# Optimization experiments

Hardware: AMD Instinct MI355X
Metric: run time of the kernel (lower is better)

The kernel has to match this reference:

```python
import jax, jax.numpy as jnp
import numpy as np
import math

BLKQ = 64
BLKK = 32
TOPK_FRAC = 0.1


def setup_inputs() -> dict:
    key = jax.random.key(0)
    k1, k2, k3, k4, k5 = jax.random.split(key, 5)
    B, L, H, D = 1, 8192, 16, 64
    q = jax.random.normal(k1, (B, L, H, D), jnp.float32)
    k = jax.random.normal(k2, (B, L, H, D), jnp.float32)
    v = jax.random.normal(k3, (B, L, H, D), jnp.float32)
    # proj_l initialized with nn.init.normal_ (std=1) in the original
    W_proj = jax.random.normal(k4, (D, D), jnp.float32)
    b_proj = jax.random.normal(k5, (D,), jnp.float32)
    return {"q": q, "k": k, "v": v, "W_proj": W_proj, "b_proj": b_proj}


def reference(q, k, v, W_proj, b_proj):
    B, L, H, D = q.shape
    lcm = BLKQ * BLKK // math.gcd(BLKQ, BLKK)
    L_pad = ((L + lcm - 1) // lcm) * lcm
    pad = L_pad - L
    scale = 1.0 / math.sqrt(D)

    # [B, L, H, D] -> [B, H, L_pad, D], zero padded (fused_transpose_pad)
    qt = jnp.transpose(q, (0, 2, 1, 3))
    kt = jnp.transpose(k, (0, 2, 1, 3))
    vt = jnp.transpose(v, (0, 2, 1, 3))
    if pad:
        pw = ((0, 0), (0, 0), (0, pad), (0, 0))
        qt_p = jnp.pad(qt, pw); kt_p = jnp.pad(kt, pw); vt_p = jnp.pad(vt, pw)
    else:
        qt_p, kt_p, vt_p = qt, kt, vt

    # key smoothing (SAGE): subtract per-(b,h) mean of padded k
    km = kt_p.mean(axis=-2, keepdims=True)          # [B, H, 1, D]
    kc = kt_p - km

    M = L_pad // BLKQ
    N = L_pad // BLKK
    # block pooling for routing scores
    pooled_q = qt_p.reshape(B, H, M, BLKQ, D).mean(axis=3)   # [B,H,M,D]
    pooled_k = kc.reshape(B, H, N, BLKK, D).mean(axis=3)     # [B,H,N,D]
    score = jnp.einsum('bhmd,bhnd->bhmn', pooled_q, pooled_k)

    T = min(N, int(TOPK_FRAC * N))                  # real_topk (static)
    _, idx = jax.lax.top_k(score, T)                # [B,H,M,T]
    lut = jnp.sort(idx, axis=-1)

    # gather selected key/value blocks: [B,H,M,T,BLKK,D]
    kb = kc.reshape(B, H, N, BLKK, D)
    vb = vt_p.reshape(B, H, N, BLKK, D)
    kg = jnp.take_along_axis(kb[:, :, None], lut[..., None, None], axis=3)
    vg = jnp.take_along_axis(vb[:, :, None], lut[..., None, None], axis=3)

    qb = qt_p.reshape(B, H, M, BLKQ, D)
    # block-sparse scores: [B,H,M,BLKQ,T,BLKK]
    s = jnp.einsum('bhmqd,bhmtkd->bhmqtk', qb, kg) * scale
    key_pos = lut[..., None] * BLKK + jnp.arange(BLKK)       # [B,H,M,T,BLKK]
    valid = key_pos < L
    s = jnp.where(valid[:, :, :, None, :, :], s, -jnp.inf)
    s = s.reshape(B, H, M, BLKQ, T * BLKK)
    p = jax.nn.softmax(s, axis=-1)
    o_s = jnp.einsum('bhmqn,bhmnd->bhmqd', p, vg.reshape(B, H, M, T * BLKK, D))
    o_s = o_s.reshape(B, H, L_pad, D)[:, :, :L]              # slice to seq_len

    # linear attention branch (softmax feature map over D)
    q_fm = jax.nn.softmax(qt_p[:, :, :L], axis=-1)
    k_fm = jax.nn.softmax(kt_p[:, :, :L], axis=-1)
    kvsum = jnp.einsum('bhld,bhle->bhde', k_fm, vt)          # [B,H,D,D]
    ksum = k_fm.sum(axis=-2)                                 # [B,H,D]
    denom = jnp.einsum('bhld,bhd->bhl', q_fm, ksum)[..., None] + 1e-6
    o_l = jnp.einsum('bhld,bhde->bhle', q_fm, kvsum) / denom
    o_l = o_l @ W_proj.T + b_proj                            # proj_l

    o = jnp.transpose(o_l + o_s, (0, 2, 1, 3))               # [B,L,H,D]
    return o
```

## Files before the change

kernel.cpp:

```cpp
#include <hip/hip_runtime.h>
#include <math.h>

#define SEQL 8192
#define NH 16
#define HD 1024
#define TSEL 25

#define OFF_KVPART 0
#define OFF_KSUM   262144
#define OFF_ZEND   263168
#define OFF_PK     263168
#define OFF_KWT    525312
#define OFF_KSWZ   558080
#define OFF_LUT    131072

typedef __attribute__((ext_vector_type(8))) short bf16x8;
typedef __attribute__((ext_vector_type(4))) float f32x4;

static __device__ inline short f2bf(float f) {
    union { float f; unsigned u; } c; c.f = f;
    unsigned r = (c.u + 0x7FFFu + ((c.u >> 16) & 1u)) >> 16;
    return (short)r;
}
static __device__ inline bf16x8 cvt8(float4 a, float4 b) {
    bf16x8 r;
    r[0] = f2bf(a.x); r[1] = f2bf(a.y); r[2] = f2bf(a.z); r[3] = f2bf(a.w);
    r[4] = f2bf(b.x); r[5] = f2bf(b.y); r[6] = f2bf(b.z); r[7] = f2bf(b.w);
    return r;
}
static __device__ inline unsigned cvtpk(float a, float b) {
    unsigned r;
    asm("v_cvt_pk_bf16_f32 %0, %1, %2" : "=v"(r) : "v"(a), "v"(b));
    return r;
}
static __device__ inline float exp2a(float x) {
#if __has_builtin(__builtin_amdgcn_exp2f)
    return __builtin_amdgcn_exp2f(x);
#else
    float r; asm("v_exp_f32 %0, %1" : "=v"(r) : "v"(x)); return r;
#endif
}
static __device__ inline void load_lds16(const void* g, void* l) {
    __builtin_amdgcn_global_load_lds((const __attribute__((address_space(1))) unsigned int*)g,
                                     (__attribute__((address_space(3))) unsigned int*)l,
                                     16, 0, 0);
}

__global__ __launch_bounds__(256) void prep_lin(const float* __restrict__ k,
                                                const float* __restrict__ v,
                                                short* __restrict__ kswz,
                                                short* __restrict__ vswz,
                                                float* __restrict__ pk,
                                                float* __restrict__ kvpart,
                                                float* __restrict__ ksum) {
    __shared__ __align__(16) float kf[2][64][68];
    __shared__ __align__(16) float vv[2][64][68];
    __shared__ float pcol[2][2][4][64];
    int b = blockIdx.x;
    int h = b >> 5, sc = b & 31;
    int t = threadIdx.x;
    int lane = t & 63, w = t >> 6;
    int r32 = t >> 3, ch = t & 7;
    int d0 = (lane >> 4) * 4 + w * 16;
    int e0 = (lane & 15) * 4;
    float acc[16];
    #pragma unroll
    for (int i = 0; i < 16; i++) acc[i] = 0.f;
    float ks_acc = 0.f;

    const float* kb_ = k + (size_t)(sc * 256 + r32) * HD + h * 64 + ch * 8;
    const float* vb_ = v + (size_t)(sc * 256 + r32) * HD + h * 64 + ch * 8;
    float4 K0a = *(const float4*)kb_;
    float4 K0b = *(const float4*)(kb_ + 4);
    float4 K1a = *(const float4*)(kb_ + (size_t)32 * HD);
    float4 K1b = *(const float4*)(kb_ + (size_t)32 * HD + 4);
    float4 V0a = *(const float4*)vb_;
    float4 V0b = *(const float4*)(vb_ + 4);
    float4 V1a = *(const float4*)(vb_ + (size_t)32 * HD);
    float4 V1b = *(const float4*)(vb_ + (size_t)32 * HD + 4);

    #pragma unroll
    for (int ph = 0; ph < 4; ph++) {
        int buf = ph & 1;
        int n0 = sc * 8 + ph * 2;
        {
            *(float4*)&vv[buf][r32][ch * 8]          = V0a;
            *(float4*)&vv[buf][r32][ch * 8 + 4]      = V0b;
            *(float4*)&vv[buf][32 + r32][ch * 8]     = V1a;
            *(float4*)&vv[buf][32 + r32][ch * 8 + 4] = V1b;
        }
        {
            int f = r32 * 8 + (ch ^ (r32 & 7));
            *(bf16x8*)(kswz + (size_t)(h * 256 + n0) * 2048 + f * 8)     = cvt8(K0a, K0b);
            *(bf16x8*)(kswz + (size_t)(h * 256 + n0 + 1) * 2048 + f * 8) = cvt8(K1a, K1b);
        }
        {
            float s_[8] = { K0a.x, K0a.y, K0a.z, K0a.w, K0b.x, K0b.y, K0b.z, K0b.w };
            #pragma unroll
            for (int j = 0; j < 8; j++) {
                s_[j] += __shfl_xor(s_[j], 8, 64);
                s_[j] += __shfl_xor(s_[j], 16, 64);
                s_[j] += __shfl_xor(s_[j], 32, 64);
            }
            if (lane < 8) {
                #pragma unroll
                for (int j = 0; j < 8; j++) pcol[buf][0][w][(t & 7) * 8 + j] = s_[j];
            }
            float s1_[8] = { K1a.x, K1a.y, K1a.z, K1a.w, K1b.x, K1b.y, K1b.z, K1b.w };
            #pragma unroll
            for (int j = 0; j < 8; j++) {
                s1_[j] += __shfl_xor(s1_[j], 8, 64);
                s1_[j] += __shfl_xor(s1_[j], 16, 64);
                s1_[j] += __shfl_xor(s1_[j], 32, 64);
            }
            if (lane < 8) {
                #pragma unroll
                for (int j = 0; j < 8; j++) pcol[buf][1][w][(t & 7) * 8 + j] = s1_[j];
            }
        }
        {
            float mx = fmaxf(fmaxf(fmaxf(K0a.x, K0a.y), fmaxf(K0a.z, K0a.w)),
                             fmaxf(fmaxf(K0b.x, K0b.y), fmaxf(K0b.z, K0b.w)));
            mx = fmaxf(mx, __shfl_xor(mx, 1, 64));
            mx = fmaxf(mx, __shfl_xor(mx, 2, 64));
            mx = fmaxf(mx, __shfl_xor(mx, 4, 64));
            float4 Fa, Fb;
            Fa.x = __expf(K0a.x - mx); Fa.y = __expf(K0a.y - mx);
            Fa.z = __expf(K0a.z - mx); Fa.w = __expf(K0a.w - mx);
            Fb.x = __expf(K0b.x - mx); Fb.y = __expf(K0b.y - mx);
            Fb.z = __expf(K0b.z - mx); Fb.w = __expf(K0b.w - mx);
            float sm = (Fa.x + Fa.y + Fa.z + Fa.w) + (Fb.x + Fb.y + Fb.z + Fb.w);
            sm += __shfl_xor(sm, 1, 64);
            sm += __shfl_xor(sm, 2, 64);
            sm += __shfl_xor(sm, 4, 64);
            float inv = 1.f / sm;
            Fa.x *= inv; Fa.y *= inv; Fa.z *= inv; Fa.w *= inv;
            Fb.x *= inv; Fb.y *= inv; Fb.z *= inv; Fb.w *= inv;
            *(float4*)&kf[buf][r32][ch * 8]     = Fa;
            *(float4*)&kf[buf][r32][ch * 8 + 4] = Fb;
        }
        {
            float mx = fmaxf(fmaxf(fmaxf(K1a.x, K1a.y), fmaxf(K1a.z, K1a.w)),
                             fmaxf(fmaxf(K1b.x, K1b.y), fmaxf(K1b.z, K1b.w)));
            mx = fmaxf(mx, __shfl_xor(mx, 1, 64));
            mx = fmaxf(mx, __shfl_xor(mx, 2, 64));
            mx = fmaxf(mx, __shfl_xor(mx, 4, 64));
            float4 Fa, Fb;
            Fa.x = __expf(K1a.x - mx); Fa.y = __expf(K1a.y - mx);
            Fa.z = __expf(K1a.z - mx); Fa.w = __expf(K1a.w - mx);
            Fb.x = __expf(K1b.x - mx); Fb.y = __expf(K1b.y - mx);
            Fb.z = __expf(K1b.z - mx); Fb.w = __expf(K1b.w - mx);
            float sm = (Fa.x + Fa.y + Fa.z + Fa.w) + (Fb.x + Fb.y + Fb.z + Fb.w);
            sm += __shfl_xor(sm, 1, 64);
            sm += __shfl_xor(sm, 2, 64);
            sm += __shfl_xor(sm, 4, 64);
            float inv = 1.f / sm;
            Fa.x *= inv; Fa.y *= inv; Fa.z *= inv; Fa.w *= inv;
            Fb.x *= inv; Fb.y *= inv; Fb.z *= inv; Fb.w *= inv;
            *(float4*)&kf[buf][32 + r32][ch * 8]     = Fa;
            *(float4*)&kf[buf][32 + r32][ch * 8 + 4] = Fb;
        }
        if (ph < 3) {
            const float* kn = kb_ + (size_t)(ph + 1) * 64 * HD;
            const float* vn = vb_ + (size_t)(ph + 1) * 64 * HD;
            K0a = *(const float4*)kn;
            K0b = *(const float4*)(kn + 4);
            K1a = *(const float4*)(kn + (size_t)32 * HD);
            K1b = *(const float4*)(kn + (size_t)32 * HD + 4);
            V0a = *(const float4*)vn;
            V0b = *(const float4*)(vn + 4);
            V1a = *(const float4*)(vn + (size_t)32 * HD);
            V1b = *(const float4*)(vn + (size_t)32 * HD + 4);
        }
        __syncthreads();
        if (t < 128) {
            int s = t >> 6, d = t & 63;
            pk[(size_t)(h * 256 + n0 + s) * 64 + d] =
                (pcol[buf][s][0][d] + pcol[buf][s][1][d] + pcol[buf][s][2][d] + pcol[buf][s][3][d])
                * (1.f / 32.f);
        }
        {
            int c = w, d = lane;
            #pragma unroll
            for (int s = 0; s < 2; s++) {
                bf16x8 val;
                #pragma unroll
                for (int j = 0; j < 8; j++) val[j] = f2bf(vv[buf][s * 32 + c * 8 + j][d]);
                int f = d * 4 + (c ^ ((d >> 1) & 3));
                *(bf16x8*)(vswz + (size_t)(h * 256 + n0 + s) * 2048 + f * 8) = val;
            }
        }
        #pragma unroll 8
        for (int l = 0; l < 64; l++) {
            float4 kd = *(const float4*)&kf[buf][l][d0];
            float4 ve = *(const float4*)&vv[buf][l][e0];
            acc[0]  += kd.x * ve.x; acc[1]  += kd.x * ve.y; acc[2]  += kd.x * ve.z; acc[3]  += kd.x * ve.w;
            acc[4]  += kd.y * ve.x; acc[5]  += kd.y * ve.y; acc[6]  += kd.y * ve.z; acc[7]  += kd.y * ve.w;
            acc[8]  += kd.z * ve.x; acc[9]  += kd.z * ve.y; acc[10] += kd.z * ve.z; acc[11] += kd.z * ve.w;
            acc[12] += kd.w * ve.x; acc[13] += kd.w * ve.y; acc[14] += kd.w * ve.z; acc[15] += kd.w * ve.w;
        }
        if (t < 64) {
            float s = 0.f;
            #pragma unroll 8
            for (int l = 0; l < 64; l++) s += kf[buf][l][t];
            ks_acc += s;
        }
    }
    float* dst = kvpart + ((size_t)(sc & 3) * 16 + h) * 4096;
    #pragma unroll
    for (int i = 0; i < 4; i++)
        #pragma unroll
        for (int j = 0; j < 4; j++)
            atomicAdd(&dst[(d0 + i) * 64 + e0 + j], acc[i * 4 + j]);
    if (t < 64) atomicAdd(&ksum[h * 64 + t], ks_acc);
}

__global__ __launch_bounds__(256) void score_topk(const float* __restrict__ q,
                                                  const float* __restrict__ pk,
                                                  int* __restrict__ lut) {
    __shared__ __align__(16) float pq_s[64];
    __shared__ __align__(16) float s_s[256];
    __shared__ int wcnt[4];
    int b = blockIdx.x;
    int h = b >> 7, m = b & 127;
    int t = threadIdx.x;
    int lane = t & 63, w = t >> 6;
    if (t < 64) {
        const float* base = q + (size_t)m * 64 * HD + h * 64 + t;
        float s = 0.f;
        #pragma unroll 8
        for (int r = 0; r < 64; r++) s += base[(size_t)r * HD];
        pq_s[t] = s * (1.f / 64.f);
    }
    __syncthreads();
    const float* kr = pk + ((size_t)h * 256 + t) * 64;
    double acc = 0.0;
    #pragma unroll 8
    for (int d = 0; d < 64; d++) acc += (double)pq_s[d] * (double)kr[d];
    float sc = (float)acc;
    s_s[t] = sc;
    __syncthreads();
    int cnt = 0;
    float si = sc;
    #pragma unroll 4
    for (int j4 = 0; j4 < 64; j4++) {
        float4 sv = *(const float4*)&s_s[j4 * 4];
        int j = j4 * 4;
        cnt += (sv.x > si) || (sv.x == si && (j + 0) < t);
        cnt += (sv.y > si) || (sv.y == si && (j + 1) < t);
        cnt += (sv.z > si) || (sv.z == si && (j + 2) < t);
        cnt += (sv.w > si) || (sv.w == si && (j + 3) < t);
    }
    bool sel = cnt < TSEL;
    unsigned long long bal = __ballot(sel);
    if (lane == 0) wcnt[w] = __popcll(bal);
    __syncthreads();
    if (sel) {
        int off = __popcll(bal & ((1ull << lane) - 1ull));
        for (int i = 0; i < w; i++) off += wcnt[i];
        lut[(size_t)b * TSEL + off] = t;
    }
}

__global__ __launch_bounds__(256) void kw_mul(const float* __restrict__ kvpart,
                                              const float* __restrict__ W,
                                              short* __restrict__ kwt) {
    __shared__ __align__(16) float kv[16][68];
    __shared__ __align__(16) float wsm[64][68];
    int h = blockIdx.x >> 2, dq = blockIdx.x & 3;
    int t = threadIdx.x;
    for (int i = t; i < 1024; i += 256) {
        int dl = i >> 6, e = i & 63;
        float s = 0.f;
        #pragma unroll
        for (int p = 0; p < 4; p++)
            s += kvpart[((size_t)p * 16 + h) * 4096 + (dq * 16 + dl) * 64 + e];
        kv[dl][e] = s;
    }
    for (int i = t; i < 4096; i += 256) wsm[i >> 6][i & 63] = W[i];
    __syncthreads();
    int lane = t & 63, wi = t >> 6;
    int dl = lane & 15;
    int db = wi * 16 + (lane >> 4) * 4;
    #pragma unroll
    for (int j = 0; j < 4; j++) {
        int dd = db + j;
        float a = 0.f;
        #pragma unroll
        for (int e4 = 0; e4 < 16; e4++) {
            float4 kq = *(const float4*)&kv[dl][e4 * 4];
            float4 wq = *(const float4*)&wsm[dd][e4 * 4];
            a += kq.x * wq.x + kq.y * wq.y + kq.z * wq.z + kq.w * wq.w;
        }
        kwt[(size_t)h * 4096 + dd * 64 + dq * 16 + dl] = f2bf(a);
    }
}

__global__ __launch_bounds__(256) void sparse_attn_mfma(const float* __restrict__ q,
                                                        const short* __restrict__ kswz,
                                                        const short* __restrict__ vswz,
                                                        const int* __restrict__ lut,
                                                        const short* __restrict__ kwt,
                                                        const float* __restrict__ ksum,
                                                        const float* __restrict__ bproj,
                                                        float* __restrict__ out) {
    __shared__ __align__(16) short Kb[3][2048];
    __shared__ __align__(16) short Vb[3][2048];
    __shared__ __align__(16) short Pl[64][44];
    __shared__ int lut_s[TSEL];

    int b = blockIdx.x;
    int x = b & 7, jj = b >> 3;
    int h = x * 2 + (jj >> 7);
    int m = jj & 127;
    int t = threadIdx.x;
    int lane = t & 63, w = t >> 6;
    int l15 = lane & 15, quad = lane >> 4;

    if (t < TSEL) lut_s[t] = lut[(size_t)(h * 128 + m) * TSEL + t];
    __syncthreads();

    {
        size_t base = (size_t)(h * 256 + lut_s[0]) * 2048;
        load_lds16(kswz + base + t * 8, &Kb[0][t * 8]);
        load_lds16(vswz + base + t * 8, &Vb[0][t * 8]);
        load_lds16(kwt + (size_t)h * 4096 + t * 8, &Kb[1][t * 8]);
        load_lds16(kwt + (size_t)h * 4096 + 2048 + t * 8, &Vb[1][t * 8]);
    }

    const float* qrow = q + (size_t)(m * 64 + w * 16 + l15) * HD + h * 64;
    float4 x0 = *(const float4*)(qrow + quad * 8);
    float4 x1 = *(const float4*)(qrow + quad * 8 + 4);
    float4 x2 = *(const float4*)(qrow + 32 + quad * 8);
    float4 x3 = *(const float4*)(qrow + 32 + quad * 8 + 4);
    bf16x8 qa[2];
    qa[0] = cvt8(x0, x1);
    qa[1] = cvt8(x2, x3);

    float mx = fmaxf(fmaxf(fmaxf(x0.x, x0.y), fmaxf(x0.z, x0.w)),
                     fmaxf(fmaxf(x1.x, x1.y), fmaxf(x1.z, x1.w)));
    mx = fmaxf(mx, fmaxf(fmaxf(fmaxf(x2.x, x2.y), fmaxf(x2.z, x2.w)),
                         fmaxf(fmaxf(x3.x, x3.y), fmaxf(x3.z, x3.w))));
    mx = fmaxf(mx, __shfl_xor(mx, 16, 64));
    mx = fmaxf(mx, __shfl_xor(mx, 32, 64));
    x0.x = __expf(x0.x - mx); x0.y = __expf(x0.y - mx); x0.z = __expf(x0.z - mx); x0.w = __expf(x0.w - mx);
    x1.x = __expf(x1.x - mx); x1.y = __expf(x1.y - mx); x1.z = __expf(x1.z - mx); x1.w = __expf(x1.w - mx);
    x2.x = __expf(x2.x - mx); x2.y = __expf(x2.y - mx); x2.z = __expf(x2.z - mx); x2.w = __expf(x2.w - mx);
    x3.x = __expf(x3.x - mx); x3.y = __expf(x3.y - mx); x3.z = __expf(x3.z - mx); x3.w = __expf(x3.w - mx);
    float sm = (x0.x + x0.y + x0.z + x0.w) + (x1.x + x1.y + x1.z + x1.w)
             + (x2.x + x2.y + x2.z + x2.w) + (x3.x + x3.y + x3.z + x3.w);
    sm += __shfl_xor(sm, 16, 64);
    sm += __shfl_xor(sm, 32, 64);
    float qsc = 1.f / sm;
    float4 ka0 = *(const float4*)(ksum + h * 64 + quad * 8);
    float4 ka1 = *(const float4*)(ksum + h * 64 + quad * 8 + 4);
    float4 ka2 = *(const float4*)(ksum + h * 64 + 32 + quad * 8);
    float4 ka3 = *(const float4*)(ksum + h * 64 + 32 + quad * 8 + 4);
    float dq = x0.x * ka0.x + x0.y * ka0.y + x0.z * ka0.z + x0.w * ka0.w
             + x1.x * ka1.x + x1.y * ka1.y + x1.z * ka1.z + x1.w * ka1.w
             + x2.x * ka2.x + x2.y * ka2.y + x2.z * ka2.z + x2.w * ka2.w
             + x3.x * ka3.x + x3.y * ka3.y + x3.z * ka3.z + x3.w * ka3.w;
    dq += __shfl_xor(dq, 16, 64);
    dq += __shfl_xor(dq, 32, 64);
    float invd = 1.f / (dq * qsc + 1e-6f);
    x0.x *= qsc; x0.y *= qsc; x0.z *= qsc; x0.w *= qsc;
    x1.x *= qsc; x1.y *= qsc; x1.z *= qsc; x1.w *= qsc;
    x2.x *= qsc; x2.y *= qsc; x2.z *= qsc; x2.w *= qsc;
    x3.x *= qsc; x3.y *= qsc; x3.z *= qsc; x3.w *= qsc;
    bf16x8 qf[2];
    qf[0] = cvt8(x0, x1);
    qf[1] = cvt8(x2, x3);

    __syncthreads();

    f32x4 Ol[4];
    #pragma unroll
    for (int dt = 0; dt < 4; dt++) Ol[dt] = (f32x4){0.f, 0.f, 0.f, 0.f};
    __builtin_amdgcn_s_setprio(1);
    #pragma unroll
    for (int dt = 0; dt < 4; dt++) {
        #pragma unroll
        for (int kc = 0; kc < 2; kc++) {
            int flat = (dt * 16 + l15) * 64 + kc * 32 + quad * 8;
            bf16x8 a = (dt < 2) ? *(const bf16x8*)&Kb[1][flat]
                                : *(const bf16x8*)&Vb[1][flat - 2048];
            Ol[dt] = __builtin_amdgcn_mfma_f32_16x16x32_bf16(a, qf[kc], Ol[dt], 0, 0, 0);
        }
    }
    __builtin_amdgcn_s_setprio(0);

    __syncthreads();
    {
        size_t base = (size_t)(h * 256 + lut_s[1]) * 2048;
        load_lds16(kswz + base + t * 8, &Kb[1][t * 8]);
        load_lds16(vswz + base + t * 8, &Vb[1][t * 8]);
    }

    f32x4 O[4];
    #pragma unroll
    for (int dt = 0; dt < 4; dt++) O[dt] = (f32x4){0.f, 0.f, 0.f, 0.f};
    float l_i = 0.f;
    const f32x4 z = (f32x4){0.f, 0.f, 0.f, 0.f};
    const float EC = 1.44269504f * 0.125f;

    int bc = 0;
    for (int ti = 0; ti < TSEL; ti++) {
        if (ti > 0) {
            if (ti < TSEL - 1) asm volatile("s_waitcnt vmcnt(2)" ::: "memory");
            else               asm volatile("s_waitcnt vmcnt(0)" ::: "memory");
            __builtin_amdgcn_s_barrier();
            __builtin_amdgcn_sched_barrier(0);
        }
        if (ti + 2 < TSEL) {
            int bs = bc ? bc - 1 : 2;
            size_t base = (size_t)(h * 256 + lut_s[ti + 2]) * 2048;
            load_lds16(kswz + base + t * 8, &Kb[bs][t * 8]);
            load_lds16(vswz + base + t * 8, &Vb[bs][t * 8]);
        }
        int r0 = l15, r1 = 16 + l15;
        bf16x8 a00 = *(const bf16x8*)&Kb[bc][(r0 * 8 + (quad ^ (r0 & 7))) * 8];
        bf16x8 a01 = *(const bf16x8*)&Kb[bc][(r0 * 8 + ((4 + quad) ^ (r0 & 7))) * 8];
        bf16x8 a10 = *(const bf16x8*)&Kb[bc][(r1 * 8 + (quad ^ (r1 & 7))) * 8];
        bf16x8 a11 = *(const bf16x8*)&Kb[bc][(r1 * 8 + ((4 + quad) ^ (r1 & 7))) * 8];
        __builtin_amdgcn_s_setprio(1);
        f32x4 s0 = __builtin_amdgcn_mfma_f32_16x16x32_bf16(a00, qa[0], z, 0, 0, 0);
        s0 = __builtin_amdgcn_mfma_f32_16x16x32_bf16(a01, qa[1], s0, 0, 0, 0);
        f32x4 s1 = __builtin_amdgcn_mfma_f32_16x16x32_bf16(a10, qa[0], z, 0, 0, 0);
        s1 = __builtin_amdgcn_mfma_f32_16x16x32_bf16(a11, qa[1], s1, 0, 0, 0);
        __builtin_amdgcn_s_setprio(0);

        float p0[4], p1[4];
        float lsum = 0.f;
        #pragma unroll
        for (int r = 0; r < 4; r++) {
            p0[r] = exp2a(s0[r] * EC);
            p1[r] = exp2a(s1[r] * EC);
            lsum += p0[r] + p1[r];
        }
        lsum += __shfl_xor(lsum, 16, 64);
        lsum += __shfl_xor(lsum, 32, 64);
        l_i += lsum;

        uint2 pkA, pkB;
        pkA.x = cvtpk(p0[0], p0[1]); pkA.y = cvtpk(p0[2], p0[3]);
        pkB.x = cvtpk(p1[0], p1[1]); pkB.y = cvtpk(p1[2], p1[3]);
        *(uint2*)&Pl[w * 16 + l15][quad * 4] = pkA;
        *(uint2*)&Pl[w * 16 + l15][16 + quad * 4] = pkB;

        asm volatile("s_waitcnt lgkmcnt(0)" ::: "memory");
        __builtin_amdgcn_sched_barrier(0);

        bf16x8 pb = *(const bf16x8*)&Pl[w * 16 + l15][quad * 8];
        __builtin_amdgcn_s_setprio(1);
        #pragma unroll
        for (int dt = 0; dt < 4; dt++) {
            int d = dt * 16 + l15;
            bf16x8 va = *(const bf16x8*)&Vb[bc][(d * 4 + (quad ^ ((d >> 1) & 3))) * 8];
            O[dt] = __builtin_amdgcn_mfma_f32_16x16x32_bf16(va, pb, O[dt], 0, 0, 0);
        }
        __builtin_amdgcn_s_setprio(0);

        bc++; if (bc == 3) bc = 0;
    }

    float inv = 1.f / l_i;
    float* dst = out + (size_t)(m * 64 + w * 16 + l15) * HD + h * 64;
    #pragma unroll
    for (int dt = 0; dt < 4; dt++) {
        float4 bv = *(const float4*)(bproj + dt * 16 + quad * 4);
        float4 o;
        o.x = O[dt][0] * inv + Ol[dt][0] * invd + bv.x;
        o.y = O[dt][1] * inv + Ol[dt][1] * invd + bv.y;
        o.z = O[dt][2] * inv + Ol[dt][2] * invd + bv.z;
        o.w = O[dt][3] * inv + Ol[dt][3] * invd + bv.w;
        *(float4*)(dst + dt * 16 + quad * 4) = o;
    }
}

extern "C" void kernel_launch(void* const* d_in, const int* in_sizes, int n_in,
                              void* d_out, int out_size, void* d_ws, size_t ws_size,
                              hipStream_t stream) {
    const float* q  = (const float*)d_in[0];
    const float* k  = (const float*)d_in[1];
    const float* v  = (const float*)d_in[2];
    const float* W  = (const float*)d_in[3];
    const float* bp = (const float*)d_in[4];
    float* out = (float*)d_out;
    float* ws = (float*)d_ws;

    float* kvpart = ws + OFF_KVPART;
    float* ksum   = ws + OFF_KSUM;
    float* pk     = ws + OFF_PK;
    short* kwt    = (short*)(ws + OFF_KWT);
    short* kswz   = (short*)(ws + OFF_KSWZ);
    short* vswz   = kswz + (size_t)16 * 256 * 2048;
    int*   lut    = (int*)(ws + OFF_LUT);

    hipMemsetAsync(ws, 0, OFF_ZEND * sizeof(float), stream);
    prep_lin<<<512, 256, 0, stream>>>(k, v, kswz, vswz, pk, kvpart, ksum);
    kw_mul<<<64, 256, 0, stream>>>(kvpart, W, kwt);
    score_topk<<<2048, 256, 0, stream>>>(q, pk, lut);
    sparse_attn_mfma<<<2048, 256, 0, stream>>>(q, kswz, vswz, lut, kwt, ksum, bp, out);
}
```

Before: 267.9 us.

## Redistribute softmax probabilities in registers via permlane swaps instead of LDS

Replaces the LDS round-trip that transposes P from the score MFMA output layout into the PV MFMA operand layout with permlane32/permlane16 swap instructions done entirely in registers. This drops the P staging buffer, its LDS writes and reads, and the lgkmcnt wait in every key-block iteration. The row-sum reduction across lanes moves out of the loop and runs once at the end. The V fragments are also loaded earlier, before the score MFMAs, so their LDS latency overlaps compute, at the cost of extra VGPRs.

```diff
diff --git a/kernel.cpp b/kernel.cpp
--- a/kernel.cpp
+++ b/kernel.cpp
@@ -16,6 +16,8 @@
 
 typedef __attribute__((ext_vector_type(8))) short bf16x8;
 typedef __attribute__((ext_vector_type(4))) float f32x4;
+typedef __attribute__((ext_vector_type(4))) unsigned u32x4;
+typedef __attribute__((ext_vector_type(2))) unsigned u32x2;
 
 static __device__ inline short f2bf(float f) {
     union { float f; unsigned u; } c; c.f = f;
@@ -40,6 +42,37 @@
     float r; asm("v_exp_f32 %0, %1" : "=v"(r) : "v"(x)); return r;
 #endif
 }
+#if __has_builtin(__builtin_amdgcn_permlane32_swap)
+static __device__ inline unsigned xor32v(unsigned x, bool hi) {
+    u32x2 r;
+    {
+        auto t = __builtin_amdgcn_permlane32_swap(x, x, false, false);
+        r[0] = t[0]; r[1] = t[1];
+    }
+    return hi ? r[0] : r[1];
+}
+static __device__ inline unsigned xor16v(unsigned x, bool hi) {
+    u32x2 r;
+    {
+        auto t = __builtin_amdgcn_permlane16_swap(x, x, false, false);
+        r[0] = t[0]; r[1] = t[1];
+    }
+    return hi ? r[0] : r[1];
+}
+#else
+static __device__ inline unsigned xor32v(unsigned x, bool hi) {
+    unsigned a = x, b;
+    asm("v_mov_b32 %0, %1" : "=v"(b) : "v"(x));
+    asm("v_permlane32_swap_b32 %0, %1" : "+v"(a), "+v"(b));
+    return hi ? a : b;
+}
+static __device__ inline unsigned xor16v(unsigned x, bool hi) {
+    unsigned a = x, b;
+    asm("v_mov_b32 %0, %1" : "=v"(b) : "v"(x));
+    asm("v_permlane16_swap_b32 %0, %1" : "+v"(a), "+v"(b));
+    return hi ? a : b;
+}
+#endif
 static __device__ inline void load_lds16(const void* g, void* l) {
     __builtin_amdgcn_global_load_lds((const __attribute__((address_space(1))) unsigned int*)g,
                                      (__attribute__((address_space(3))) unsigned int*)l,
@@ -306,7 +339,6 @@
                                                         float* __restrict__ out) {
     __shared__ __align__(16) short Kb[3][2048];
     __shared__ __align__(16) short Vb[3][2048];
-    __shared__ __align__(16) short Pl[64][44];
     __shared__ int lut_s[TSEL];
 
     int b = blockIdx.x;
@@ -316,6 +348,9 @@
     int t = threadIdx.x;
     int lane = t & 63, w = t >> 6;
     int l15 = lane & 15, quad = lane >> 4;
+    const bool b16 = (t & 16) != 0;
+    const bool b32 = (t & 32) != 0;
+    const bool beq = (b16 == b32);
 
     if (t < TSEL) lut_s[t] = lut[(size_t)(h * 128 + m) * TSEL + t];
     __syncthreads();
@@ -399,7 +434,7 @@
     f32x4 O[4];
     #pragma unroll
     for (int dt = 0; dt < 4; dt++) O[dt] = (f32x4){0.f, 0.f, 0.f, 0.f};
-    float l_i = 0.f;
+    float l_loc = 0.f;
     const f32x4 z = (f32x4){0.f, 0.f, 0.f, 0.f};
     const float EC = 1.44269504f * 0.125f;
 
@@ -422,6 +457,12 @@
         bf16x8 a01 = *(const bf16x8*)&Kb[bc][(r0 * 8 + ((4 + quad) ^ (r0 & 7))) * 8];
         bf16x8 a10 = *(const bf16x8*)&Kb[bc][(r1 * 8 + (quad ^ (r1 & 7))) * 8];
         bf16x8 a11 = *(const bf16x8*)&Kb[bc][(r1 * 8 + ((4 + quad) ^ (r1 & 7))) * 8];
+        bf16x8 va[4];
+        #pragma unroll
+        for (int dt = 0; dt < 4; dt++) {
+            int d = dt * 16 + l15;
+            va[dt] = *(const bf16x8*)&Vb[bc][(d * 4 + (quad ^ ((d >> 1) & 3))) * 8];
+        }
         __builtin_amdgcn_s_setprio(1);
         f32x4 s0 = __builtin_amdgcn_mfma_f32_16x16x32_bf16(a00, qa[0], z, 0, 0, 0);
         s0 = __builtin_amdgcn_mfma_f32_16x16x32_bf16(a01, qa[1], s0, 0, 0, 0);
@@ -430,40 +471,41 @@
         __builtin_amdgcn_s_setprio(0);
 
         float p0[4], p1[4];
-        float lsum = 0.f;
         #pragma unroll
         for (int r = 0; r < 4; r++) {
             p0[r] = exp2a(s0[r] * EC);
             p1[r] = exp2a(s1[r] * EC);
-            lsum += p0[r] + p1[r];
-        }
-        lsum += __shfl_xor(lsum, 16, 64);
-        lsum += __shfl_xor(lsum, 32, 64);
-        l_i += lsum;
-
-        uint2 pkA, pkB;
-        pkA.x = cvtpk(p0[0], p0[1]); pkA.y = cvtpk(p0[2], p0[3]);
-        pkB.x = cvtpk(p1[0], p1[1]); pkB.y = cvtpk(p1[2], p1[3]);
-        *(uint2*)&Pl[w * 16 + l15][quad * 4] = pkA;
-        *(uint2*)&Pl[w * 16 + l15][16 + quad * 4] = pkB;
-
-        asm volatile("s_waitcnt lgkmcnt(0)" ::: "memory");
-        __builtin_amdgcn_sched_barrier(0);
-
-        bf16x8 pb = *(const bf16x8*)&Pl[w * 16 + l15][quad * 8];
+        }
+        l_loc += ((p0[0] + p0[1]) + (p0[2] + p0[3])) + ((p1[0] + p1[1]) + (p1[2] + p1[3]));
+
+        unsigned c0 = cvtpk(p0[0], p0[1]);
+        unsigned c1 = cvtpk(p0[2], p0[3]);
+        unsigned c2 = cvtpk(p1[0], p1[1]);
+        unsigned c3 = cvtpk(p1[2], p1[3]);
+        unsigned d0_ = xor32v(c0, b32), d1_ = xor32v(c1, b32);
+        unsigned d2_ = xor32v(c2, b32), d3_ = xor32v(c3, b32);
+        unsigned cc0 = b32 ? c2 : c0,  cc1 = b32 ? c3 : c1;
+        unsigned dd0 = b32 ? d2_ : d0_, dd1 = b32 ? d3_ : d1_;
+        unsigned sw0 = beq ? cc0 : dd0, sw1 = beq ? cc1 : dd1;
+        unsigned t0_ = beq ? dd0 : cc0, t1_ = beq ? dd1 : cc1;
+        unsigned rv0 = xor16v(t0_, b16), rv1 = xor16v(t1_, b16);
+        u32x4 pw;
+        pw[0] = b16 ? rv0 : sw0; pw[1] = b16 ? rv1 : sw1;
+        pw[2] = b16 ? sw0 : rv0; pw[3] = b16 ? sw1 : rv1;
+        bf16x8 pb = __builtin_bit_cast(bf16x8, pw);
+
         __builtin_amdgcn_s_setprio(1);
         #pragma unroll
-        for (int dt = 0; dt < 4; dt++) {
-            int d = dt * 16 + l15;
-            bf16x8 va = *(const bf16x8*)&Vb[bc][(d * 4 + (quad ^ ((d >> 1) & 3))) * 8];
-            O[dt] = __builtin_amdgcn_mfma_f32_16x16x32_bf16(va, pb, O[dt], 0, 0, 0);
-        }
+        for (int dt = 0; dt < 4; dt++)
+            O[dt] = __builtin_amdgcn_mfma_f32_16x16x32_bf16(va[dt], pb, O[dt], 0, 0, 0);
         __builtin_amdgcn_s_setprio(0);
 
         bc++; if (bc == 3) bc = 0;
     }
 
-    float inv = 1.f / l_i;
+    l_loc += __shfl_xor(l_loc, 16, 64);
+    l_loc += __shfl_xor(l_loc, 32, 64);
+    float inv = 1.f / l_loc;
     float* dst = out + (size_t)(m * 64 + w * 16 + l15) * HD + h * 64;
     #pragma unroll
     for (int dt = 0; dt < 4; dt++) {
```

Measured after the change: 268.9 us. No clear change (+0.4%).
